# Optimization experiments

Measured on AMD Instinct MI355X. Metric: run time of the kernel, lower is better.

## Reference

```python
import jax, jax.numpy as jnp
import numpy as np

TEMPERATURE = 0.07


def setup_inputs() -> dict:
    key = jax.random.key(0)
    k1, k2, k3 = jax.random.split(key, 3)
    B, V, D = 512, 1, 512
    features = jax.random.normal(k1, (B, V, D), dtype=jnp.float32)
    mask = jax.random.randint(k2, (B, B), 0, 2).astype(jnp.float32)
    mask_sents = jax.random.randint(k3, (B,), 0, 2).astype(jnp.bool_)
    return {"features": features, "mask": mask, "mask_sents": mask_sents}


def reference(features, mask, mask_sents):
    # features: [B, 1, D]; mask: [B, B] (0/1); mask_sents: [B] bool anchor selector
    B = features.shape[0]
    anchor = features[:, 0]                     # contrast_count == 1 -> anchor == contrast
    sim = jnp.matmul(anchor, anchor.T) / TEMPERATURE   # [B, B]

    logits_mask = 1.0 - jnp.eye(B, dtype=sim.dtype)    # zero out self-comparison
    sel = mask_sents.astype(sim.dtype)[:, None]        # weight instead of boolean row-select
    mask_pos = mask * logits_mask * sel                # [B, B]
    mask_neg = (1.0 - mask) * logits_mask * sel        # [B, B]

    # 'pre' branch: sum over rows i and (pos p, neg n) pairs of -logsigmoid(sim[i,p]-sim[i,n])
    diff = sim[:, :, None] - sim[:, None, :]           # [B, P, N] pairwise differences
    neg_logsig = -jax.nn.log_sigmoid(diff)
    loss_sum = jnp.einsum('ipn,ip,in->', neg_logsig, mask_pos, mask_neg)
    pair_num = jnp.sum(mask_pos.sum(1) * mask_neg.sum(1))
    loss = jnp.where(pair_num > 0, loss_sum / jnp.maximum(pair_num, 1.0), loss_sum)
    return loss
```

## Files before the change

### kernel.cpp

```cpp
#include <hip/hip_runtime.h>
#include <hip/hip_bf16.h>
#include <math.h>

#define BDIM 512
#define DDIM 512
#define SPLIT 4

typedef __attribute__((ext_vector_type(8))) short bfrag;
typedef __attribute__((ext_vector_type(4))) float ffrag;

__global__ __launch_bounds__(256) void convert_bf16(const float* __restrict__ A,
                                                    __hip_bfloat16* __restrict__ Ab,
                                                    double* __restrict__ acc) {
    const int idx = (blockIdx.x * 256 + threadIdx.x) * 4;
    if (idx == 0) { acc[0] = 0.0; acc[1] = 0.0; }
    float4 v = *(const float4*)&A[idx];
    union { __hip_bfloat16 h[4]; ushort4 u; } cv;
    cv.h[0] = __float2bfloat16(v.x); cv.h[1] = __float2bfloat16(v.y);
    cv.h[2] = __float2bfloat16(v.z); cv.h[3] = __float2bfloat16(v.w);
    *(ushort4*)&Ab[idx] = cv.u;
}

__global__ __launch_bounds__(256) void gemm_mfma(const __hip_bfloat16* __restrict__ Ab,
                                                 float* __restrict__ S) {
    const int tid = threadIdx.x;
    const int w = tid >> 6, lane = tid & 63;
    const int quad = lane >> 4, r = lane & 15;
    const int m0 = blockIdx.y * 64 + w * 16;
    const int n0 = blockIdx.x * 16;
    const __hip_bfloat16* arow = Ab + (m0 + r) * DDIM + quad * 8;
    const __hip_bfloat16* brow = Ab + (n0 + r) * DDIM + quad * 8;
    ffrag acc = {0.f, 0.f, 0.f, 0.f};
#pragma unroll
    for (int k = 0; k < DDIM; k += 32) {
        bfrag af = *(const bfrag*)(arow + k);
        bfrag bf = *(const bfrag*)(brow + k);
        acc = __builtin_amdgcn_mfma_f32_16x16x32_bf16(af, bf, acc, 0, 0, 0);
    }
    const float sc = 1.0f / 0.07f;
#pragma unroll
    for (int rg = 0; rg < 4; ++rg)
        S[(m0 + quad * 4 + rg) * BDIM + n0 + r] = acc[rg] * sc;
}

__device__ __forceinline__ float softplus_f(float z) {
    return fmaxf(z, 0.0f) + __logf(1.0f + __expf(-fabsf(z)));
}

__global__ __launch_bounds__(256) void pair_loss(const float* __restrict__ S,
                                                 const float* __restrict__ mask,
                                                 const int* __restrict__ sel,
                                                 double* __restrict__ acc) {
    const int i = blockIdx.x >> 2;
    const int q = blockIdx.x & 3;
    if (sel[i] == 0) return;
    __shared__ float sm[BDIM];
    __shared__ __align__(16) float ps[BDIM + 4];
    __shared__ float ns[BDIM];
    __shared__ int cnt[2];
    __shared__ float wsum[4];
    const int tid = threadIdx.x;
    const int lane = tid & 63, wave = tid >> 6;
    if (tid < 2) cnt[tid] = 0;
    for (int p = tid; p < BDIM; p += 256) sm[p] = S[i * BDIM + p];
    __syncthreads();
#pragma unroll
    for (int r = 0; r < 2; ++r) {
        const int p = tid + r * 256;
        const float m = mask[i * BDIM + p];
        const bool ok  = (p != i);
        const bool isp = ok && (m != 0.0f);
        const bool isn = ok && (m == 0.0f);
        unsigned long long bp = __ballot(isp);
        unsigned long long bn = __ballot(isn);
        unsigned long long lower = (1ULL << lane) - 1ULL;
        int pbase = 0, nbase = 0;
        if (lane == 0) {
            pbase = atomicAdd(&cnt[0], __popcll(bp));
            nbase = atomicAdd(&cnt[1], __popcll(bn));
        }
        pbase = __shfl(pbase, 0, 64);
        nbase = __shfl(nbase, 0, 64);
        if (isp) ps[pbase + __popcll(bp & lower)] = sm[p];
        if (isn) ns[nbase + __popcll(bn & lower)] = sm[p];
    }
    __syncthreads();
    const int npos = cnt[0], nneg = cnt[1];
    if (tid < 4) ps[npos + tid] = INFINITY;
    __syncthreads();
    int p0 = (q == 0) ? 0 : min(npos, ((q * npos) / SPLIT + 3) & ~3);
    int p1 = (q == SPLIT - 1) ? npos : min(npos, (((q + 1) * npos) / SPLIT + 3) & ~3);
    float l0 = 0.f, l1 = 0.f, l2 = 0.f, l3 = 0.f;
    for (int pp = p0; pp < p1; pp += 4) {
        float4 sp = *(const float4*)&ps[pp];
        for (int nn = tid; nn < nneg; nn += 256) {
            float sn = ns[nn];
            l0 += softplus_f(sn - sp.x);
            l1 += softplus_f(sn - sp.y);
            l2 += softplus_f(sn - sp.z);
            l3 += softplus_f(sn - sp.w);
        }
    }
    float local = (l0 + l1) + (l2 + l3);
#pragma unroll
    for (int off = 32; off > 0; off >>= 1) local += __shfl_down(local, off, 64);
    if (lane == 0) wsum[wave] = local;
    __syncthreads();
    if (tid == 0) {
        double tot = (double)wsum[0] + (double)wsum[1] + (double)wsum[2] + (double)wsum[3];
        atomicAdd(&acc[0], tot);
        if (q == 0) atomicAdd(&acc[1], (double)npos * (double)nneg);
    }
}

__global__ void finalize(const double* __restrict__ acc, float* __restrict__ out) {
    double ls = acc[0], pn = acc[1];
    double loss = (pn > 0.0) ? ls / fmax(pn, 1.0) : ls;
    out[0] = (float)loss;
}

extern "C" void kernel_launch(void* const* d_in, const int* in_sizes, int n_in,
                              void* d_out, int out_size, void* d_ws, size_t ws_size,
                              hipStream_t stream) {
    const float* feat = (const float*)d_in[0];
    const float* mask = (const float*)d_in[1];
    const int*   sel  = (const int*)d_in[2];
    float* out = (float*)d_out;

    char* ws = (char*)d_ws;
    float* S = (float*)ws;
    double* acc = (double*)(ws + BDIM * BDIM * sizeof(float));
    __hip_bfloat16* Ab = (__hip_bfloat16*)(ws + BDIM * BDIM * 4 + 1024);

    convert_bf16<<<BDIM * DDIM / 1024, 256, 0, stream>>>(feat, Ab, acc);
    gemm_mfma<<<dim3(BDIM / 16, BDIM / 64), 256, 0, stream>>>(Ab, S);
    pair_loss<<<BDIM * SPLIT, 256, 0, stream>>>(S, mask, sel, acc);
    finalize<<<1, 1, 0, stream>>>(acc, out);
}
```

Baseline: 89.15 us.

## Fuse bf16 conversion into GEMM, finalize into pair_loss, register-held negatives

Drops the separate bf16 conversion kernel by converting fp32 features to bf16 inside the MFMA GEMM loads. It also removes the finalize kernel with a last-block-done atomic counter in pair_loss. The inner loop now keeps two negative values per thread in registers, padding unused slots with -inf so softplus adds zero, and streams over positives. This cuts two kernel launches and the shared-memory reloads of negatives, at the cost of redundant fp32 loads and conversions in the GEMM and a threadfence plus atomic per block.

Measured after the change: 196.4 us. 2.2x slower.

```diff
diff --git a/kernel.cpp b/kernel.cpp
--- a/kernel.cpp
+++ b/kernel.cpp
@@ -9,38 +9,42 @@
 typedef __attribute__((ext_vector_type(8))) short bfrag;
 typedef __attribute__((ext_vector_type(4))) float ffrag;
 
-__global__ __launch_bounds__(256) void convert_bf16(const float* __restrict__ A,
-                                                    __hip_bfloat16* __restrict__ Ab,
-                                                    double* __restrict__ acc) {
-    const int idx = (blockIdx.x * 256 + threadIdx.x) * 4;
-    if (idx == 0) { acc[0] = 0.0; acc[1] = 0.0; }
-    float4 v = *(const float4*)&A[idx];
-    union { __hip_bfloat16 h[4]; ushort4 u; } cv;
-    cv.h[0] = __float2bfloat16(v.x); cv.h[1] = __float2bfloat16(v.y);
-    cv.h[2] = __float2bfloat16(v.z); cv.h[3] = __float2bfloat16(v.w);
-    *(ushort4*)&Ab[idx] = cv.u;
+__device__ __forceinline__ bfrag load_cvt8(const float* __restrict__ p) {
+    float4 u = *(const float4*)p;
+    float4 v = *(const float4*)(p + 4);
+    union { __hip_bfloat16 h[8]; bfrag f; } cv;
+    cv.h[0] = __float2bfloat16(u.x); cv.h[1] = __float2bfloat16(u.y);
+    cv.h[2] = __float2bfloat16(u.z); cv.h[3] = __float2bfloat16(u.w);
+    cv.h[4] = __float2bfloat16(v.x); cv.h[5] = __float2bfloat16(v.y);
+    cv.h[6] = __float2bfloat16(v.z); cv.h[7] = __float2bfloat16(v.w);
+    return cv.f;
 }
 
-__global__ __launch_bounds__(256) void gemm_mfma(const __hip_bfloat16* __restrict__ Ab,
-                                                 float* __restrict__ S) {
+__global__ __launch_bounds__(256) void gemm_mfma(const float* __restrict__ A,
+                                                 float* __restrict__ S,
+                                                 double* __restrict__ acc,
+                                                 unsigned* __restrict__ ctr) {
+    if (blockIdx.x == 0 && blockIdx.y == 0 && threadIdx.x == 0) {
+        acc[0] = 0.0; acc[1] = 0.0; *ctr = 0u;
+    }
     const int tid = threadIdx.x;
     const int w = tid >> 6, lane = tid & 63;
     const int quad = lane >> 4, r = lane & 15;
     const int m0 = blockIdx.y * 64 + w * 16;
     const int n0 = blockIdx.x * 16;
-    const __hip_bfloat16* arow = Ab + (m0 + r) * DDIM + quad * 8;
-    const __hip_bfloat16* brow = Ab + (n0 + r) * DDIM + quad * 8;
-    ffrag acc = {0.f, 0.f, 0.f, 0.f};
+    const float* arow = A + (m0 + r) * DDIM + quad * 8;
+    const float* brow = A + (n0 + r) * DDIM + quad * 8;
+    ffrag c = {0.f, 0.f, 0.f, 0.f};
 #pragma unroll
     for (int k = 0; k < DDIM; k += 32) {
-        bfrag af = *(const bfrag*)(arow + k);
-        bfrag bf = *(const bfrag*)(brow + k);
-        acc = __builtin_amdgcn_mfma_f32_16x16x32_bf16(af, bf, acc, 0, 0, 0);
+        bfrag af = load_cvt8(arow + k);
+        bfrag bf = load_cvt8(brow + k);
+        c = __builtin_amdgcn_mfma_f32_16x16x32_bf16(af, bf, c, 0, 0, 0);
     }
     const float sc = 1.0f / 0.07f;
 #pragma unroll
     for (int rg = 0; rg < 4; ++rg)
-        S[(m0 + quad * 4 + rg) * BDIM + n0 + r] = acc[rg] * sc;
+        S[(m0 + quad * 4 + rg) * BDIM + n0 + r] = c[rg] * sc;
 }
 
 __device__ __forceinline__ float softplus_f(float z) {
@@ -50,73 +54,86 @@
 __global__ __launch_bounds__(256) void pair_loss(const float* __restrict__ S,
                                                  const float* __restrict__ mask,
                                                  const int* __restrict__ sel,
-                                                 double* __restrict__ acc) {
+                                                 double* __restrict__ acc,
+                                                 unsigned* __restrict__ ctr,
+                                                 float* __restrict__ out) {
     const int i = blockIdx.x >> 2;
     const int q = blockIdx.x & 3;
-    if (sel[i] == 0) return;
-    __shared__ float sm[BDIM];
-    __shared__ __align__(16) float ps[BDIM + 4];
-    __shared__ float ns[BDIM];
-    __shared__ int cnt[2];
-    __shared__ float wsum[4];
     const int tid = threadIdx.x;
     const int lane = tid & 63, wave = tid >> 6;
-    if (tid < 2) cnt[tid] = 0;
-    for (int p = tid; p < BDIM; p += 256) sm[p] = S[i * BDIM + p];
-    __syncthreads();
+    const bool active = (sel[i] != 0);
+    if (active) {
+        __shared__ float sm[BDIM];
+        __shared__ __align__(16) float ps[BDIM + 4];
+        __shared__ float ns[BDIM];
+        __shared__ int cnt[2];
+        __shared__ float wsum[4];
+        if (tid < 2) cnt[tid] = 0;
+        *(float2*)&sm[tid * 2] = *(const float2*)&S[i * BDIM + tid * 2];
+        __syncthreads();
 #pragma unroll
-    for (int r = 0; r < 2; ++r) {
-        const int p = tid + r * 256;
-        const float m = mask[i * BDIM + p];
-        const bool ok  = (p != i);
-        const bool isp = ok && (m != 0.0f);
-        const bool isn = ok && (m == 0.0f);
-        unsigned long long bp = __ballot(isp);
-        unsigned long long bn = __ballot(isn);
-        unsigned long long lower = (1ULL << lane) - 1ULL;
-        int pbase = 0, nbase = 0;
-        if (lane == 0) {
-            pbase = atomicAdd(&cnt[0], __popcll(bp));
-            nbase = atomicAdd(&cnt[1], __popcll(bn));
+        for (int rr = 0; rr < 2; ++rr) {
+            const int p = tid + rr * 256;
+            const float m = mask[i * BDIM + p];
+            const bool ok  = (p != i);
+            const bool isp = ok && (m != 0.0f);
+            const bool isn = ok && (m == 0.0f);
+            unsigned long long bp = __ballot(isp);
+            unsigned long long bn = __ballot(isn);
+            unsigned long long lower = (1ULL << lane) - 1ULL;
+            int pbase = 0, nbase = 0;
+            if (lane == 0) {
+                pbase = atomicAdd(&cnt[0], __popcll(bp));
+                nbase = atomicAdd(&cnt[1], __popcll(bn));
+            }
+            pbase = __shfl(pbase, 0, 64);
+            nbase = __shfl(nbase, 0, 64);
+            if (isp) ps[pbase + __popcll(bp & lower)] = sm[p];
+            if (isn) ns[nbase + __popcll(bn & lower)] = sm[p];
         }
-        pbase = __shfl(pbase, 0, 64);
-        nbase = __shfl(nbase, 0, 64);
-        if (isp) ps[pbase + __popcll(bp & lower)] = sm[p];
-        if (isn) ns[nbase + __popcll(bn & lower)] = sm[p];
-    }
-    __syncthreads();
-    const int npos = cnt[0], nneg = cnt[1];
-    if (tid < 4) ps[npos + tid] = INFINITY;
-    __syncthreads();
-    int p0 = (q == 0) ? 0 : min(npos, ((q * npos) / SPLIT + 3) & ~3);
-    int p1 = (q == SPLIT - 1) ? npos : min(npos, (((q + 1) * npos) / SPLIT + 3) & ~3);
-    float l0 = 0.f, l1 = 0.f, l2 = 0.f, l3 = 0.f;
-    for (int pp = p0; pp < p1; pp += 4) {
-        float4 sp = *(const float4*)&ps[pp];
-        for (int nn = tid; nn < nneg; nn += 256) {
-            float sn = ns[nn];
-            l0 += softplus_f(sn - sp.x);
-            l1 += softplus_f(sn - sp.y);
-            l2 += softplus_f(sn - sp.z);
-            l3 += softplus_f(sn - sp.w);
+        __syncthreads();
+        const int npos = cnt[0], nneg = cnt[1];
+        if (tid < 4) ps[npos + tid] = INFINITY;
+        for (int x = nneg + tid; x < BDIM; x += 256) ns[x] = -INFINITY;
+        __syncthreads();
+        const float sn0 = ns[tid];
+        const float sn1 = ns[tid + 256];
+        int p0 = (q == 0) ? 0 : min(npos, ((q * npos) / SPLIT + 3) & ~3);
+        int p1 = (q == SPLIT - 1) ? npos : min(npos, (((q + 1) * npos) / SPLIT + 3) & ~3);
+        float l0 = 0.f, l1 = 0.f, l2 = 0.f, l3 = 0.f;
+        float l4 = 0.f, l5 = 0.f, l6 = 0.f, l7 = 0.f;
+        for (int pp = p0; pp < p1; pp += 4) {
+            float4 sp = *(const float4*)&ps[pp];
+            l0 += softplus_f(sn0 - sp.x);
+            l1 += softplus_f(sn0 - sp.y);
+            l2 += softplus_f(sn0 - sp.z);
+            l3 += softplus_f(sn0 - sp.w);
+            l4 += softplus_f(sn1 - sp.x);
+            l5 += softplus_f(sn1 - sp.y);
+            l6 += softplus_f(sn1 - sp.z);
+            l7 += softplus_f(sn1 - sp.w);
+        }
+        float local = ((l0 + l1) + (l2 + l3)) + ((l4 + l5) + (l6 + l7));
+#pragma unroll
+        for (int off = 32; off > 0; off >>= 1) local += __shfl_down(local, off, 64);
+        if (lane == 0) wsum[wave] = local;
+        __syncthreads();
+        if (tid == 0) {
+            double tot = (double)wsum[0] + (double)wsum[1] + (double)wsum[2] + (double)wsum[3];
+            atomicAdd(&acc[0], tot);
+            if (q == 0) atomicAdd(&acc[1], (double)npos * (double)nneg);
         }
     }
-    float local = (l0 + l1) + (l2 + l3);
-#pragma unroll
-    for (int off = 32; off > 0; off >>= 1) local += __shfl_down(local, off, 64);
-    if (lane == 0) wsum[wave] = local;
-    __syncthreads();
+    __threadfence();
     if (tid == 0) {
-        double tot = (double)wsum[0] + (double)wsum[1] + (double)wsum[2] + (double)wsum[3];
-        atomicAdd(&acc[0], tot);
-        if (q == 0) atomicAdd(&acc[1], (double)npos * (double)nneg);
+        unsigned done = atomicAdd(ctr, 1u);
+        if (done == gridDim.x - 1) {
+            __threadfence();
+            double ls = acc[0], pn = acc[1];
+            double loss = (pn > 0.0) ? ls / fmax(pn, 1.0) : ls;
+            out[0] = (float)loss;
+        }
     }
-}
-
-__global__ void finalize(const double* __restrict__ acc, float* __restrict__ out) {
-    double ls = acc[0], pn = acc[1];
-    double loss = (pn > 0.0) ? ls / fmax(pn, 1.0) : ls;
-    out[0] = (float)loss;
 }
 
 extern "C" void kernel_launch(void* const* d_in, const int* in_sizes, int n_in,
@@ -130,10 +147,8 @@
     char* ws = (char*)d_ws;
     float* S = (float*)ws;
     double* acc = (double*)(ws + BDIM * BDIM * sizeof(float));
-    __hip_bfloat16* Ab = (__hip_bfloat16*)(ws + BDIM * BDIM * 4 + 1024);
+    unsigned* ctr = (unsigned*)(ws + BDIM * BDIM * sizeof(float) + 16);
 
-    convert_bf16<<<BDIM * DDIM / 1024, 256, 0, stream>>>(feat, Ab, acc);
-    gemm_mfma<<<dim3(BDIM / 16, BDIM / 64), 256, 0, stream>>>(Ab, S);
-    pair_loss<<<BDIM * SPLIT, 256, 0, stream>>>(S, mask, sel, acc);
-    finalize<<<1, 1, 0, stream>>>(acc, out);
+    gemm_mfma<<<dim3(BDIM / 16, BDIM / 64), 256, 0, stream>>>(feat, S, acc, ctr);
+    pair_loss<<<BDIM * SPLIT, 256, 0, stream>>>(S, mask, sel, acc, ctr, out);
 }
```
